# Optimization experiments

Hardware: AMD Instinct MI355X
Metric: run time of the kernel (lower is better)

Reference implementation:

```python
import jax, jax.numpy as jnp
import numpy as np

ENTITY_NUM = 500000
RELATION_NUM = 1000
DIM = 256
BATCH = 16384
MARGIN = 1.0
EPS = 1e-6  # torch.nn.PairwiseDistance default eps, added to the difference


def setup_inputs() -> dict:
    key = jax.random.key(0)
    ks = jax.random.split(key, 10)
    entity_emb = jax.random.normal(ks[0], (ENTITY_NUM, DIM), jnp.float32) * 0.1
    entity_map_emb = jax.random.normal(ks[1], (ENTITY_NUM, DIM), jnp.float32) * 0.1
    rel_emb = jax.random.normal(ks[2], (RELATION_NUM, DIM), jnp.float32) * 0.1
    rel_map_emb = jax.random.normal(ks[3], (RELATION_NUM, DIM), jnp.float32) * 0.1

    def make_triples(kh, kr, kt):
        h = jax.random.randint(kh, (BATCH, 1), 0, ENTITY_NUM, jnp.int64)
        r = jax.random.randint(kr, (BATCH, 1), 0, RELATION_NUM, jnp.int64)
        t = jax.random.randint(kt, (BATCH, 1), 0, ENTITY_NUM, jnp.int64)
        return jnp.concatenate([h, r, t], axis=1)

    pos_x = make_triples(ks[4], ks[5], ks[6])
    neg_x = make_triples(ks[7], ks[8], ks[9])
    return {
        "pos_x": pos_x,
        "neg_x": neg_x,
        "entity_emb": entity_emb,
        "entity_map_emb": entity_map_emb,
        "rel_emb": rel_emb,
        "rel_map_emb": rel_map_emb,
    }


def _score(tri, entity_emb, entity_map_emb, rel_emb, rel_map_emb):
    # tri: [B, 3] = (head, relation, tail)
    h_idx, r_idx, t_idx = tri[:, 0], tri[:, 1], tri[:, 2]
    h = entity_emb[h_idx]          # [B, D]
    hp = entity_map_emb[h_idx]     # [B, D]
    t = entity_emb[t_idx]          # [B, D]
    tp = entity_map_emb[t_idx]     # [B, D]
    r = rel_emb[r_idx]             # [B, D]
    rp = rel_map_emb[r_idx]        # [B, D]
    # Mrh = rp hp^T + I  =>  Mrh @ h = rp * (hp . h) + h  (rank-1 update, same math,
    # avoids materializing [B, D, D])
    h_proj = rp * jnp.sum(hp * h, axis=-1, keepdims=True) + h
    t_proj = rp * jnp.sum(tp * t, axis=-1, keepdims=True) + t
    diff = h_proj + r - t_proj + EPS  # PairwiseDistance adds eps to the difference
    return jnp.sqrt(jnp.sum(diff * diff, axis=-1))  # [B]


def reference(pos_x, neg_x, entity_emb, entity_map_emb, rel_emb, rel_map_emb):
    pos_score = _score(pos_x, entity_emb, entity_map_emb, rel_emb, rel_map_emb)
    neg_score = _score(neg_x, entity_emb, entity_map_emb, rel_emb, rel_map_emb)
    b = pos_x.shape[0]
    return jnp.sum(jax.nn.relu(pos_score - neg_score + MARGIN)) / b
```

## Files before the change

kernel.cpp:

```cpp
#include <hip/hip_runtime.h>
#include <stdint.h>

#define DIM 256
#define BATCH 16384
#define MARGIN 1.0f
#define EPSV 1e-6f

#define PPB 8
#define NBLOCKS (BATCH / PPB)

typedef float fx4 __attribute__((ext_vector_type(4)));

__device__ __forceinline__ float dot4(fx4 a, fx4 b) {
    return a.x * b.x + a.y * b.y + a.z * b.z + a.w * b.w;
}

__device__ __forceinline__ void gload_lds16(const void* g, void* l) {
    __builtin_amdgcn_global_load_lds(
        (const __attribute__((address_space(1))) uint32_t*)g,
        (__attribute__((address_space(3))) uint32_t*)l, 16, 0, 0);
}

__global__ __launch_bounds__(256, 2) void transd_loss_kernel(
    const int* __restrict__ pos_x, const int* __restrict__ neg_x,
    const float* __restrict__ ent, const float* __restrict__ entm,
    const float* __restrict__ rel, const float* __restrict__ relm,
    float* __restrict__ partial) {
    __shared__ float rows[64 * DIM];
    __shared__ float wsum[4];

    const int tid  = threadIdx.x;
    const int w    = tid >> 6;
    const int lane = tid & 63;
    const int g0   = blockIdx.x * PPB;

    int hidx[2][2], ridx[2][2], tidx[2][2];
#pragma unroll
    for (int p2 = 0; p2 < 2; ++p2) {
        const int p = 2 * w + p2;
#pragma unroll
        for (int s = 0; s < 2; ++s) {
            const int* __restrict__ tri = s ? neg_x : pos_x;
            hidx[p2][s] = tri[(g0 + p) * 3 + 0];
            ridx[p2][s] = tri[(g0 + p) * 3 + 1];
            tidx[p2][s] = tri[(g0 + p) * 3 + 2];
        }
    }

    const int lf = lane * 4;
#pragma unroll
    for (int p2 = 0; p2 < 2; ++p2) {
        const int p = 2 * w + p2;
#pragma unroll
        for (int s = 0; s < 2; ++s) {
            float* rb = &rows[(p * 8 + s * 4) * DIM];
            const size_t ho = (size_t)hidx[p2][s] * DIM + lf;
            const size_t to = (size_t)tidx[p2][s] * DIM + lf;
            gload_lds16(ent  + ho, rb + 0 * DIM);
            gload_lds16(entm + ho, rb + 1 * DIM);
            gload_lds16(ent  + to, rb + 2 * DIM);
            gload_lds16(entm + to, rb + 3 * DIM);
        }
    }

    fx4 rv[2][2], rpv[2][2];
#pragma unroll
    for (int p2 = 0; p2 < 2; ++p2) {
#pragma unroll
        for (int s = 0; s < 2; ++s) {
            const size_t ro = (size_t)ridx[p2][s] * DIM + lf;
            rv[p2][s]  = *(const fx4*)(rel  + ro);
            rpv[p2][s] = *(const fx4*)(relm + ro);
        }
    }

    __syncthreads();

    float acc = 0.0f;
#pragma unroll
    for (int p2 = 0; p2 < 2; ++p2) {
        const int p  = 2 * w + p2;
        const float* rb0 = &rows[(p * 8 + 0) * DIM];
        const float* rb1 = &rows[(p * 8 + 4) * DIM];
        fx4 h0  = *(const fx4*)(rb0 + 0 * DIM + lf);
        fx4 hp0 = *(const fx4*)(rb0 + 1 * DIM + lf);
        fx4 t0  = *(const fx4*)(rb0 + 2 * DIM + lf);
        fx4 tp0 = *(const fx4*)(rb0 + 3 * DIM + lf);
        fx4 h1  = *(const fx4*)(rb1 + 0 * DIM + lf);
        fx4 hp1 = *(const fx4*)(rb1 + 1 * DIM + lf);
        fx4 t1  = *(const fx4*)(rb1 + 2 * DIM + lf);
        fx4 tp1 = *(const fx4*)(rb1 + 3 * DIM + lf);

        float a0 = dot4(h0, hp0), b0 = dot4(t0, tp0);
        float a1 = dot4(h1, hp1), b1 = dot4(t1, tp1);
#pragma unroll
        for (int m = 32; m > 0; m >>= 1) {
            a0 += __shfl_xor(a0, m, 64);
            b0 += __shfl_xor(b0, m, 64);
            a1 += __shfl_xor(a1, m, 64);
            b1 += __shfl_xor(b1, m, 64);
        }
        const float ab0 = a0 - b0, ab1 = a1 - b1;

        fx4 d0 = rpv[p2][0] * ab0 + h0 + rv[p2][0] - t0 + EPSV;
        fx4 d1 = rpv[p2][1] * ab1 + h1 + rv[p2][1] - t1 + EPSV;
        float ss0 = dot4(d0, d0), ss1 = dot4(d1, d1);
#pragma unroll
        for (int m = 32; m > 0; m >>= 1) {
            ss0 += __shfl_xor(ss0, m, 64);
            ss1 += __shfl_xor(ss1, m, 64);
        }
        const float v = sqrtf(ss0) - sqrtf(ss1) + MARGIN;
        acc += v > 0.0f ? v : 0.0f;
    }

    if (lane == 0) wsum[w] = acc;
    __syncthreads();
    if (tid == 0) partial[blockIdx.x] = (wsum[0] + wsum[1]) + (wsum[2] + wsum[3]);
}

__global__ __launch_bounds__(256) void reduce_kernel(const float* __restrict__ partial,
                                                     float* __restrict__ out) {
    const int lane = threadIdx.x & 63;
    float s = 0.0f;
    for (int i = threadIdx.x; i < NBLOCKS; i += 256) s += partial[i];
#pragma unroll
    for (int m = 32; m > 0; m >>= 1) s += __shfl_xor(s, m, 64);
    __shared__ float smem[4];
    if (lane == 0) smem[threadIdx.x >> 6] = s;
    __syncthreads();
    if (threadIdx.x == 0)
        out[0] = ((smem[0] + smem[1]) + (smem[2] + smem[3])) / (float)BATCH;
}

extern "C" void kernel_launch(void* const* d_in, const int* in_sizes, int n_in,
                              void* d_out, int out_size, void* d_ws, size_t ws_size,
                              hipStream_t stream) {
    const int*   pos_x = (const int*)d_in[0];
    const int*   neg_x = (const int*)d_in[1];
    const float* ent   = (const float*)d_in[2];
    const float* entm  = (const float*)d_in[3];
    const float* rel   = (const float*)d_in[4];
    const float* relm  = (const float*)d_in[5];

    float* partial = (float*)d_ws;
    float* out     = (float*)d_out;

    transd_loss_kernel<<<NBLOCKS, 256, 0, stream>>>(pos_x, neg_x, ent, entm, rel, relm, partial);
    reduce_kernel<<<1, 256, 0, stream>>>(partial, out);
}
```

Baseline: 35.01 us.

## Double-buffer per-wave gathers across eight pairs with async LDS prefetch

Each wave now handles eight triple pairs in a loop instead of two. Gathers for the next pair are issued into a second LDS stage while the current pair is computed, using explicit vmcnt waits and no block barrier. The grid shrinks from 2048 to 512 blocks. This trades raw parallelism, and with it the number of concurrent memory requests, for in-wave overlap, and correctness relies on the hand-counted vmcnt values.

```diff
diff --git a/kernel.cpp b/kernel.cpp
--- a/kernel.cpp
+++ b/kernel.cpp
@@ -6,8 +6,11 @@
 #define MARGIN 1.0f
 #define EPSV 1e-6f
 
-#define PPB 8
-#define NBLOCKS (BATCH / PPB)
+#define WPB 4
+#define PPW 8
+#define MAIN_BLOCKS (BATCH / (WPB * PPW))
+#define STAGE_FLOATS (8 * DIM)
+#define WAVE_LDS (2 * STAGE_FLOATS)
 
 typedef float fx4 __attribute__((ext_vector_type(4)));
 
@@ -21,75 +24,84 @@
         (__attribute__((address_space(3))) uint32_t*)l, 16, 0, 0);
 }
 
+#define WAITV(n) asm volatile("s_waitcnt vmcnt(" #n ")" ::: "memory")
+
 __global__ __launch_bounds__(256, 2) void transd_loss_kernel(
     const int* __restrict__ pos_x, const int* __restrict__ neg_x,
     const float* __restrict__ ent, const float* __restrict__ entm,
     const float* __restrict__ rel, const float* __restrict__ relm,
     float* __restrict__ partial) {
-    __shared__ float rows[64 * DIM];
-    __shared__ float wsum[4];
+    __shared__ float rows[WPB * WAVE_LDS];
+    __shared__ float wsum[WPB];
 
     const int tid  = threadIdx.x;
     const int w    = tid >> 6;
     const int lane = tid & 63;
-    const int g0   = blockIdx.x * PPB;
+    const int lf   = lane * 4;
+    const int p0   = (blockIdx.x * WPB + w) * PPW;
+    float* wbuf = &rows[w * WAVE_LDS];
 
-    int hidx[2][2], ridx[2][2], tidx[2][2];
-#pragma unroll
-    for (int p2 = 0; p2 < 2; ++p2) {
-        const int p = 2 * w + p2;
-#pragma unroll
-        for (int s = 0; s < 2; ++s) {
-            const int* __restrict__ tri = s ? neg_x : pos_x;
-            hidx[p2][s] = tri[(g0 + p) * 3 + 0];
-            ridx[p2][s] = tri[(g0 + p) * 3 + 1];
-            tidx[p2][s] = tri[(g0 + p) * 3 + 2];
-        }
-    }
+    int ph[2], pr[2], pt[2], nh[2], nr[2], nt[2];
+    fx4 rv[2][2], rpv[2][2];
 
-    const int lf = lane * 4;
-#pragma unroll
-    for (int p2 = 0; p2 < 2; ++p2) {
-        const int p = 2 * w + p2;
-#pragma unroll
-        for (int s = 0; s < 2; ++s) {
-            float* rb = &rows[(p * 8 + s * 4) * DIM];
-            const size_t ho = (size_t)hidx[p2][s] * DIM + lf;
-            const size_t to = (size_t)tidx[p2][s] * DIM + lf;
-            gload_lds16(ent  + ho, rb + 0 * DIM);
-            gload_lds16(entm + ho, rb + 1 * DIM);
-            gload_lds16(ent  + to, rb + 2 * DIM);
-            gload_lds16(entm + to, rb + 3 * DIM);
-        }
-    }
+#define LOAD_IDX(b, j) do {                                              \
+        const int p_ = p0 + (j);                                         \
+        ph[b] = pos_x[p_ * 3 + 0];                                       \
+        pr[b] = pos_x[p_ * 3 + 1];                                       \
+        pt[b] = pos_x[p_ * 3 + 2];                                       \
+        nh[b] = neg_x[p_ * 3 + 0];                                       \
+        nr[b] = neg_x[p_ * 3 + 1];                                       \
+        nt[b] = neg_x[p_ * 3 + 2];                                       \
+    } while (0)
 
-    fx4 rv[2][2], rpv[2][2];
-#pragma unroll
-    for (int p2 = 0; p2 < 2; ++p2) {
-#pragma unroll
-        for (int s = 0; s < 2; ++s) {
-            const size_t ro = (size_t)ridx[p2][s] * DIM + lf;
-            rv[p2][s]  = *(const fx4*)(rel  + ro);
-            rpv[p2][s] = *(const fx4*)(relm + ro);
-        }
-    }
+#define ISSUE_STAGE(b) do {                                              \
+        float* sb_ = wbuf + (b) * STAGE_FLOATS;                          \
+        const size_t hop = (size_t)ph[b] * DIM + lf;                     \
+        const size_t top = (size_t)pt[b] * DIM + lf;                     \
+        const size_t hon = (size_t)nh[b] * DIM + lf;                     \
+        const size_t ton = (size_t)nt[b] * DIM + lf;                     \
+        gload_lds16(ent  + hop, sb_ + 0 * DIM);                          \
+        gload_lds16(entm + hop, sb_ + 1 * DIM);                          \
+        gload_lds16(ent  + top, sb_ + 2 * DIM);                          \
+        gload_lds16(entm + top, sb_ + 3 * DIM);                          \
+        gload_lds16(ent  + hon, sb_ + 4 * DIM);                          \
+        gload_lds16(entm + hon, sb_ + 5 * DIM);                          \
+        gload_lds16(ent  + ton, sb_ + 6 * DIM);                          \
+        gload_lds16(entm + ton, sb_ + 7 * DIM);                          \
+        const size_t rop = (size_t)pr[b] * DIM + lf;                     \
+        const size_t ron = (size_t)nr[b] * DIM + lf;                     \
+        rv[b][0]  = *(const fx4*)(rel  + rop);                           \
+        rpv[b][0] = *(const fx4*)(relm + rop);                           \
+        rv[b][1]  = *(const fx4*)(rel  + ron);                           \
+        rpv[b][1] = *(const fx4*)(relm + ron);                           \
+    } while (0)
 
-    __syncthreads();
+    LOAD_IDX(0, 0);
+    LOAD_IDX(1, 1);
+    ISSUE_STAGE(0);
 
     float acc = 0.0f;
 #pragma unroll
-    for (int p2 = 0; p2 < 2; ++p2) {
-        const int p  = 2 * w + p2;
-        const float* rb0 = &rows[(p * 8 + 0) * DIM];
-        const float* rb1 = &rows[(p * 8 + 4) * DIM];
-        fx4 h0  = *(const fx4*)(rb0 + 0 * DIM + lf);
-        fx4 hp0 = *(const fx4*)(rb0 + 1 * DIM + lf);
-        fx4 t0  = *(const fx4*)(rb0 + 2 * DIM + lf);
-        fx4 tp0 = *(const fx4*)(rb0 + 3 * DIM + lf);
-        fx4 h1  = *(const fx4*)(rb1 + 0 * DIM + lf);
-        fx4 hp1 = *(const fx4*)(rb1 + 1 * DIM + lf);
-        fx4 t1  = *(const fx4*)(rb1 + 2 * DIM + lf);
-        fx4 tp1 = *(const fx4*)(rb1 + 3 * DIM + lf);
+    for (int j = 0; j < PPW; ++j) {
+        const int cb = j & 1;
+        const int nb = (j + 1) & 1;
+        if (j + 2 < PPW) LOAD_IDX(cb, j + 2);
+        if (j + 1 < PPW) ISSUE_STAGE(nb);
+
+        if (j <= PPW - 3)      { WAITV(18); }
+        else if (j == PPW - 2) { WAITV(12); }
+        else                   { WAITV(0);  }
+        __builtin_amdgcn_sched_barrier(0);
+
+        const float* sb = wbuf + cb * STAGE_FLOATS;
+        fx4 h0  = *(const fx4*)(sb + 0 * DIM + lf);
+        fx4 hp0 = *(const fx4*)(sb + 1 * DIM + lf);
+        fx4 t0  = *(const fx4*)(sb + 2 * DIM + lf);
+        fx4 tp0 = *(const fx4*)(sb + 3 * DIM + lf);
+        fx4 h1  = *(const fx4*)(sb + 4 * DIM + lf);
+        fx4 hp1 = *(const fx4*)(sb + 5 * DIM + lf);
+        fx4 t1  = *(const fx4*)(sb + 6 * DIM + lf);
+        fx4 tp1 = *(const fx4*)(sb + 7 * DIM + lf);
 
         float a0 = dot4(h0, hp0), b0 = dot4(t0, tp0);
         float a1 = dot4(h1, hp1), b1 = dot4(t1, tp1);
@@ -102,8 +114,8 @@
         }
         const float ab0 = a0 - b0, ab1 = a1 - b1;
 
-        fx4 d0 = rpv[p2][0] * ab0 + h0 + rv[p2][0] - t0 + EPSV;
-        fx4 d1 = rpv[p2][1] * ab1 + h1 + rv[p2][1] - t1 + EPSV;
+        fx4 d0 = rpv[cb][0] * ab0 + h0 + rv[cb][0] - t0 + EPSV;
+        fx4 d1 = rpv[cb][1] * ab1 + h1 + rv[cb][1] - t1 + EPSV;
         float ss0 = dot4(d0, d0), ss1 = dot4(d1, d1);
 #pragma unroll
         for (int m = 32; m > 0; m >>= 1) {
@@ -113,17 +125,20 @@
         const float v = sqrtf(ss0) - sqrtf(ss1) + MARGIN;
         acc += v > 0.0f ? v : 0.0f;
     }
+#undef LOAD_IDX
+#undef ISSUE_STAGE
 
     if (lane == 0) wsum[w] = acc;
     __syncthreads();
-    if (tid == 0) partial[blockIdx.x] = (wsum[0] + wsum[1]) + (wsum[2] + wsum[3]);
+    if (tid == 0)
+        partial[blockIdx.x] = (wsum[0] + wsum[1]) + (wsum[2] + wsum[3]);
 }
 
 __global__ __launch_bounds__(256) void reduce_kernel(const float* __restrict__ partial,
                                                      float* __restrict__ out) {
     const int lane = threadIdx.x & 63;
     float s = 0.0f;
-    for (int i = threadIdx.x; i < NBLOCKS; i += 256) s += partial[i];
+    for (int i = threadIdx.x; i < MAIN_BLOCKS; i += 256) s += partial[i];
 #pragma unroll
     for (int m = 32; m > 0; m >>= 1) s += __shfl_xor(s, m, 64);
     __shared__ float smem[4];
@@ -146,6 +161,6 @@
     float* partial = (float*)d_ws;
     float* out     = (float*)d_out;
 
-    transd_loss_kernel<<<NBLOCKS, 256, 0, stream>>>(pos_x, neg_x, ent, entm, rel, relm, partial);
+    transd_loss_kernel<<<MAIN_BLOCKS, 256, 0, stream>>>(pos_x, neg_x, ent, entm, rel, relm, partial);
     reduce_kernel<<<1, 256, 0, stream>>>(partial, out);
 }
```

After: 34.38 us (median of 2 runs). About the same (-1.8%).
